# Optimization experiments

Hardware: AMD Instinct MI355X
Metric: run time of the kernel (lower is better)

## Reference

```python
import jax, jax.numpy as jnp
import numpy as np


def _safe_sqrt(x):
    # cdist-style euclidean distance with grad-safe sqrt at 0
    return jnp.sqrt(jnp.maximum(x, 1e-12))


def setup_inputs() -> dict:
    key = jax.random.key(0)
    k1, k2, k3 = jax.random.split(key, 3)
    B, P, D, C, N = 256, 196, 768, 15, 12544
    return {
        "query_features": jax.random.normal(k1, (B, P, D), dtype=jnp.float32),
        "keys": jax.random.normal(k2, (C, P, D), dtype=jnp.float32),
        "embeddings": jax.random.normal(k3, (N, D), dtype=jnp.float32),
        "num_samples": 196,
    }


def _retrieve_key(query_features, keys):
    # torch.cdist(new_flat.unsqueeze(1), keys_flat.unsqueeze(0)).squeeze(1); min over classes
    B = query_features.shape[0]
    C = keys.shape[0]
    q = query_features.reshape(B, -1)  # [B, P*D]
    k = keys.reshape(C, -1)            # [C, P*D]
    sq = (jnp.sum(q * q, axis=1)[:, None]
          + jnp.sum(k * k, axis=1)[None, :]
          - 2.0 * (q @ k.T))           # [B, C] squared distances via GEMM
    d = _safe_sqrt(sq)
    min_dist = jnp.min(d, axis=1)
    min_idx = jnp.argmin(d, axis=1)
    return min_dist, min_idx


def _fps(embeddings, num_samples):
    # furthest_point_sampling_embeddings: iterative cdist-to-last-centroid,
    # running min of distances, argmax picks next centroid.
    # (torch version seeds with a random index; we use index 0 deterministically)
    N = embeddings.shape[0]
    sqn = jnp.sum(embeddings * embeddings, axis=1)  # [N]

    def step(carry, _):
        dists, last = carry
        c = embeddings[last]                          # [D]
        cur = _safe_sqrt(sqn - 2.0 * (embeddings @ c) + jnp.sum(c * c))
        dists = jnp.minimum(dists, cur)
        nxt = jnp.argmax(dists).astype(jnp.int32)
        return (dists, nxt), nxt

    init = (jnp.full((N,), jnp.inf, dtype=embeddings.dtype), jnp.int32(0))
    _, idxs = jax.lax.scan(step, init, None, length=num_samples - 1)
    idxs = jnp.concatenate([jnp.zeros((1,), dtype=idxs.dtype), idxs])
    return embeddings[idxs]  # [num_samples, D]


def reference(query_features, keys, embeddings, num_samples):
    min_dist, min_idx = _retrieve_key(query_features, keys)
    samples = _fps(embeddings, num_samples)
    return min_dist, min_idx, samples
```

## Files before the change

kernel.cpp:

```cpp
#include <hip/hip_runtime.h>
#include <math.h>

typedef unsigned long long u64;
typedef unsigned int u32;

#define L_TOT  150528
#define ROW4   37632
#define NCHUNK 7
#define CH4    5376
#define R_ITERS 84
#define NBT    32
#define BTILE  8
#define NCLS   15

#define N_E    12544
#define DIM    768
#define NBLK   256
#define PPB    49
#define NSAMP  196
#define EPB    (PPB*DIM)
#define RSTRIDE 16

__device__ __forceinline__ float wave_sum(float v) {
#pragma unroll
  for (int m = 1; m < 64; m <<= 1) v += __shfl_xor(v, m, 64);
  return v;
}

__device__ __forceinline__ u64 wave_max_u64(u64 v) {
#pragma unroll
  for (int m = 1; m < 64; m <<= 1) {
    u64 o = __shfl_xor(v, m, 64);
    if (o > v) v = o;
  }
  return v;
}

__global__ __launch_bounds__(256) void retrieve_partial(
    const float* __restrict__ q, const float* __restrict__ k,
    float* __restrict__ part, float* __restrict__ kkpart) {
  const int bt = blockIdx.x;
  const int lc = blockIdx.y;
  const int tid = threadIdx.x;
  const int w = tid >> 6, lane = tid & 63;
  const int cbase = w * 4;
  const int ccnt = (w == 3) ? 3 : 4;
  const float4* qf = (const float4*)q;
  const float4* kf = (const float4*)k;
  const int fbase = lc * CH4 + lane;

  float acc[BTILE][4];
  float qq[BTILE];
  float kkv[4];
#pragma unroll
  for (int b = 0; b < BTILE; ++b) {
    qq[b] = 0.f;
#pragma unroll
    for (int c = 0; c < 4; ++c) acc[b][c] = 0.f;
  }
#pragma unroll
  for (int c = 0; c < 4; ++c) kkv[c] = 0.f;

  for (int it = 0; it < R_ITERS; ++it) {
    const int f = fbase + it * 64;
    float4 kv[4];
#pragma unroll
    for (int c = 0; c < 4; ++c)
      if (c < ccnt) kv[c] = kf[(size_t)(cbase + c) * ROW4 + f];
    if (bt == 0) {
#pragma unroll
      for (int c = 0; c < 4; ++c)
        if (c < ccnt)
          kkv[c] += kv[c].x*kv[c].x + kv[c].y*kv[c].y + kv[c].z*kv[c].z + kv[c].w*kv[c].w;
    }
#pragma unroll
    for (int b = 0; b < BTILE; ++b) {
      float4 qv = qf[(size_t)(bt * BTILE + b) * ROW4 + f];
#pragma unroll
      for (int c = 0; c < 4; ++c)
        if (c < ccnt)
          acc[b][c] += qv.x*kv[c].x + qv.y*kv[c].y + qv.z*kv[c].z + qv.w*kv[c].w;
      if (w == 3)
        qq[b] += qv.x*qv.x + qv.y*qv.y + qv.z*qv.z + qv.w*qv.w;
    }
  }

  const size_t pb = (size_t)(lc * NBT + bt) * 16;
#pragma unroll
  for (int b = 0; b < BTILE; ++b) {
#pragma unroll
    for (int c = 0; c < 4; ++c) {
      float v = wave_sum(acc[b][c]);
      if (lane == 0 && c < ccnt) part[(pb + cbase + c) * 8 + b] = v;
    }
    if (w == 3) {
      float v = wave_sum(qq[b]);
      if (lane == 0) part[(pb + 15) * 8 + b] = v;
    }
  }
  if (bt == 0) {
#pragma unroll
    for (int c = 0; c < 4; ++c) {
      float v = wave_sum(kkv[c]);
      if (lane == 0 && c < ccnt) kkpart[lc * 16 + cbase + c] = v;
    }
  }
}

__global__ __launch_bounds__(256) void retrieve_reduce(
    const float* __restrict__ part, const float* __restrict__ kkpart,
    float* __restrict__ out) {
  __shared__ float kn[NCLS];
  const int t = threadIdx.x;
  if (t < NCLS) {
    float s = 0.f;
    for (int lc = 0; lc < NCHUNK; ++lc) s += kkpart[lc * 16 + t];
    kn[t] = s;
  }
  __syncthreads();
  const int bt = t >> 3, bi = t & 7;
  float qq = 0.f;
  for (int lc = 0; lc < NCHUNK; ++lc)
    qq += part[((size_t)(lc * NBT + bt) * 16 + 15) * 8 + bi];
  float dmin = INFINITY;
  int didx = 0;
  for (int c = 0; c < NCLS; ++c) {
    float dot = 0.f;
    for (int lc = 0; lc < NCHUNK; ++lc)
      dot += part[((size_t)(lc * NBT + bt) * 16 + c) * 8 + bi];
    float d2 = qq + kn[c] - 2.f * dot;
    float d = sqrtf(fmaxf(d2, 1e-12f));
    if (d < dmin) { dmin = d; didx = c; }
  }
  out[t] = dmin;
  out[256 + t] = (float)didx;
}

__global__ __launch_bounds__(1024, 4) void fps_kernel(
    const float* __restrict__ emb,
    u64* __restrict__ words,
    u64* __restrict__ res8,
    float* __restrict__ out_samples) {
  extern __shared__ float e_lds[];
  const int tid = threadIdx.x;
  const int blk = blockIdx.x;
  const int w = tid >> 6, lane = tid & 63;
  const int q4 = lane >> 4;
  const int r = lane & 15;
  const int pl = w * 4 + q4;
  const bool valid = pl < PPB;
  const int p = valid ? pl : 0;

  __shared__ int hist[NSAMP];
  __shared__ u64 wkey[16];
  __shared__ u64 swin[4];

  {
    const float* src = emb + (size_t)blk * EPB;
    for (int i = tid; i < EPB; i += 1024) e_lds[i] = src[i];
  }
  __syncthreads();

  const float4* ef = (const float4*)(e_lds + (size_t)p * DIM);
  float sq;
  {
    float ss = 0.f;
#pragma unroll
    for (int jj = 0; jj < 12; ++jj) {
      float4 v = ef[r + jj * 16];
      ss = fmaf(v.x, v.x, ss); ss = fmaf(v.y, v.y, ss);
      ss = fmaf(v.z, v.z, ss); ss = fmaf(v.w, v.w, ss);
    }
#pragma unroll
    for (int m = 1; m < 16; m <<= 1) ss += __shfl_xor(ss, m, 64);
    sq = ss;
  }
  float dist2 = INFINITY;
  int last = 0;
  if (tid == 0) hist[0] = 0;
  __syncthreads();

  for (int s = 1; s < NSAMP; ++s) {
    const int buf = (s & 1) * NBLK;

    const float4* cf = (const float4*)(emb + (size_t)last * DIM);
    float4 cv[12];
#pragma unroll
    for (int jj = 0; jj < 12; ++jj) cv[jj] = cf[r + jj * 16];

    float a = 0.f, cn = 0.f;
#pragma unroll
    for (int jj = 0; jj < 12; ++jj) {
      float4 e4 = ef[r + jj * 16];
      float4 c4 = cv[jj];
      a = fmaf(e4.x, c4.x, a); a = fmaf(e4.y, c4.y, a);
      a = fmaf(e4.z, c4.z, a); a = fmaf(e4.w, c4.w, a);
      cn = fmaf(c4.x, c4.x, cn); cn = fmaf(c4.y, c4.y, cn);
      cn = fmaf(c4.z, c4.z, cn); cn = fmaf(c4.w, c4.w, cn);
    }
#pragma unroll
    for (int m = 1; m < 16; m <<= 1) {
      a += __shfl_xor(a, m, 64);
      cn += __shfl_xor(cn, m, 64);
    }

    u64 key = 0ull;
    if (valid) {
      float d2 = sq - 2.f * a + cn;
      if (d2 < dist2) dist2 = d2;
      key = ((u64)__float_as_uint(dist2) << 32) |
            (u32)(~(u32)(blk * PPB + pl));
    }
#pragma unroll
    for (int m = 16; m < 64; m <<= 1) {
      u64 o = __shfl_xor(key, m, 64);
      if (o > key) key = o;
    }
    if (lane == 0) wkey[w] = key;
    __syncthreads();

    if (w == 0) {
      u64 k = wkey[lane & 15];
#pragma unroll
      for (int m = 1; m < 16; m <<= 1) {
        u64 o = __shfl_xor(k, m, 64);
        if (o > k) k = o;
      }
      if (lane == 0) {
        const u32 bidx = ~(u32)(k & 0xffffffffull);
        const u32 bdist = (u32)(k >> 32);
        const u64 word = ((u64)s << 48) | ((u64)bdist << 16) | (u64)bidx;
        __hip_atomic_store(&words[buf + blk], word, __ATOMIC_RELAXED,
                           __HIP_MEMORY_SCOPE_AGENT);
      }
    }

    if (blk == 0) {
      if (tid < NBLK) {
        u64 w64;
        for (;;) {
          w64 = __hip_atomic_load(&words[buf + tid], __ATOMIC_RELAXED,
                                  __HIP_MEMORY_SCOPE_AGENT);
          if ((w64 >> 48) >= (u64)s) break;
        }
        u64 kk = (((w64 >> 16) & 0xffffffffull) << 32) |
                 (u64)(u32)(~(u32)(w64 & 0xffffull));
        kk = wave_max_u64(kk);
        if (lane == 0) swin[w] = kk;
      }
      __syncthreads();
      if (tid == 0) {
        u64 m = swin[0];
#pragma unroll
        for (int qi = 1; qi < 4; ++qi) if (swin[qi] > m) m = swin[qi];
        const int widx = (int)(~(u32)(m & 0xffffffffull));
        hist[s] = widx;
        const u64 rw = ((u64)s << 32) | (u32)widx;
#pragma unroll
        for (int c = 0; c < 8; ++c)
          __hip_atomic_store(&res8[(size_t)c * RSTRIDE], rw,
                             __ATOMIC_RELAXED, __HIP_MEMORY_SCOPE_AGENT);
      }
      __syncthreads();
    } else {
      if (tid == 0) {
        const u64* rp = &res8[(size_t)(blk & 7) * RSTRIDE];
        u64 r0, r1, r2, r3, rr;
        for (;;) {
          r0 = __hip_atomic_load(rp, __ATOMIC_RELAXED,
                                 __HIP_MEMORY_SCOPE_AGENT);
          r1 = __hip_atomic_load(rp, __ATOMIC_RELAXED,
                                 __HIP_MEMORY_SCOPE_AGENT);
          r2 = __hip_atomic_load(rp, __ATOMIC_RELAXED,
                                 __HIP_MEMORY_SCOPE_AGENT);
          r3 = __hip_atomic_load(rp, __ATOMIC_RELAXED,
                                 __HIP_MEMORY_SCOPE_AGENT);
          if ((r3 >> 32) >= (u64)s) { rr = r3; break; }
          if ((r2 >> 32) >= (u64)s) { rr = r2; break; }
          if ((r1 >> 32) >= (u64)s) { rr = r1; break; }
          if ((r0 >> 32) >= (u64)s) { rr = r0; break; }
        }
        hist[s] = (int)(u32)(rr & 0xffffffffull);
      }
      __syncthreads();
    }
    last = hist[s];
  }

  if (blk < NSAMP) {
    const int idx = hist[blk];
    const float4* src = (const float4*)(emb + (size_t)idx * DIM);
    float4* dst = (float4*)(out_samples + (size_t)blk * DIM);
    if (tid < DIM / 4) dst[tid] = src[tid];
  }
}

extern "C" void kernel_launch(void* const* d_in, const int* in_sizes, int n_in,
                              void* d_out, int out_size, void* d_ws, size_t ws_size,
                              hipStream_t stream) {
  const float* q   = (const float*)d_in[0];
  const float* k   = (const float*)d_in[1];
  const float* emb = (const float*)d_in[2];
  float* out = (float*)d_out;

  u64* words = (u64*)d_ws;
  u64* res8  = (u64*)((char*)d_ws + 4096);
  float* part   = (float*)((char*)d_ws + 8192);
  float* kkpart = part + 28672;

  hipMemsetAsync(d_ws, 0, 8192, stream);

  hipLaunchKernelGGL(retrieve_partial, dim3(NBT, NCHUNK), dim3(256), 0, stream,
                     q, k, part, kkpart);
  hipLaunchKernelGGL(retrieve_reduce, dim3(1), dim3(256), 0, stream,
                     part, kkpart, out);

  hipFuncSetAttribute((const void*)fps_kernel,
                      hipFuncAttributeMaxDynamicSharedMemorySize,
                      EPB * sizeof(float));

  float* samples = out + 512;
  void* args[] = {(void*)&emb, (void*)&words, (void*)&res8, (void*)&samples};
  hipLaunchCooperativeKernel((void*)fps_kernel, dim3(NBLK), dim3(1024), args,
                             EPB * sizeof(float), stream);
}
```

Baseline: 872.2 us.

## Replace per-step workgroup barriers in FPS with sequence-tagged LDS flag polling

```diff
diff --git a/kernel.cpp b/kernel.cpp
--- a/kernel.cpp
+++ b/kernel.cpp
@@ -34,6 +34,17 @@
     if (o > v) v = o;
   }
   return v;
+}
+
+__device__ __forceinline__ u64 key_from_word(u64 w) {
+  return (((w >> 16) & 0xffffffffull) << 32) |
+         (u64)(u32)(~(u32)(w & 0xffffull));
+}
+
+__device__ __forceinline__ u64 word_from_key(u64 s, u64 k) {
+  const u32 bidx = ~(u32)(k & 0xffffffffull);
+  const u32 bdist = (u32)(k >> 32);
+  return (s << 48) | ((u64)bdist << 16) | (u64)bidx;
 }
 
 __global__ __launch_bounds__(256) void retrieve_partial(
@@ -152,12 +163,21 @@
   const int p = valid ? pl : 0;
 
   __shared__ int hist[NSAMP];
-  __shared__ u64 wkey[16];
-  __shared__ u64 swin[4];
+  __shared__ u64 wkey[2][16];
+  __shared__ u64 swin[2][4];
+  __shared__ u64 lres[2];
 
   {
     const float* src = emb + (size_t)blk * EPB;
     for (int i = tid; i < EPB; i += 1024) e_lds[i] = src[i];
+  }
+  if (tid == 0) {
+    hist[0] = 0;
+#pragma unroll
+    for (int i = 0; i < 16; ++i) { wkey[0][i] = 0ull; wkey[1][i] = 0ull; }
+#pragma unroll
+    for (int i = 0; i < 4; ++i) { swin[0][i] = 0ull; swin[1][i] = 0ull; }
+    lres[0] = 0ull; lres[1] = 0ull;
   }
   __syncthreads();
 
@@ -177,11 +197,10 @@
   }
   float dist2 = INFINITY;
   int last = 0;
-  if (tid == 0) hist[0] = 0;
-  __syncthreads();
 
   for (int s = 1; s < NSAMP; ++s) {
-    const int buf = (s & 1) * NBLK;
+    const int par = s & 1;
+    const int buf = par * NBLK;
 
     const float4* cf = (const float4*)(emb + (size_t)last * DIM);
     float4 cv[12];
@@ -216,23 +235,30 @@
       u64 o = __shfl_xor(key, m, 64);
       if (o > key) key = o;
     }
-    if (lane == 0) wkey[w] = key;
-    __syncthreads();
+
+    if (lane == 0)
+      __hip_atomic_store(&wkey[par][w], word_from_key((u64)s, key),
+                         __ATOMIC_RELAXED, __HIP_MEMORY_SCOPE_WORKGROUP);
 
     if (w == 0) {
-      u64 k = wkey[lane & 15];
+      u64 kw = 0ull;
+      if (lane < 16) {
+        u64 t64;
+        for (;;) {
+          t64 = __hip_atomic_load(&wkey[par][lane], __ATOMIC_RELAXED,
+                                  __HIP_MEMORY_SCOPE_WORKGROUP);
+          if ((t64 >> 48) >= (u64)s) break;
+        }
+        kw = key_from_word(t64);
+      }
 #pragma unroll
       for (int m = 1; m < 16; m <<= 1) {
-        u64 o = __shfl_xor(k, m, 64);
-        if (o > k) k = o;
-      }
-      if (lane == 0) {
-        const u32 bidx = ~(u32)(k & 0xffffffffull);
-        const u32 bdist = (u32)(k >> 32);
-        const u64 word = ((u64)s << 48) | ((u64)bdist << 16) | (u64)bidx;
-        __hip_atomic_store(&words[buf + blk], word, __ATOMIC_RELAXED,
-                           __HIP_MEMORY_SCOPE_AGENT);
-      }
+        u64 o = __shfl_xor(kw, m, 64);
+        if (o > kw) kw = o;
+      }
+      if (lane == 0)
+        __hip_atomic_store(&words[buf + blk], word_from_key((u64)s, kw),
+                           __ATOMIC_RELAXED, __HIP_MEMORY_SCOPE_AGENT);
     }
 
     if (blk == 0) {
@@ -243,25 +269,39 @@
                                   __HIP_MEMORY_SCOPE_AGENT);
           if ((w64 >> 48) >= (u64)s) break;
         }
-        u64 kk = (((w64 >> 16) & 0xffffffffull) << 32) |
-                 (u64)(u32)(~(u32)(w64 & 0xffffull));
-        kk = wave_max_u64(kk);
-        if (lane == 0) swin[w] = kk;
-      }
-      __syncthreads();
-      if (tid == 0) {
-        u64 m = swin[0];
-#pragma unroll
-        for (int qi = 1; qi < 4; ++qi) if (swin[qi] > m) m = swin[qi];
-        const int widx = (int)(~(u32)(m & 0xffffffffull));
-        hist[s] = widx;
+        u64 kk = wave_max_u64(key_from_word(w64));
+        if (lane == 0)
+          __hip_atomic_store(&swin[par][w], word_from_key((u64)s, kk),
+                             __ATOMIC_RELAXED, __HIP_MEMORY_SCOPE_WORKGROUP);
+      }
+      if (w == 0) {
+        u64 sw = 0ull;
+        if (lane < 4) {
+          u64 t64;
+          for (;;) {
+            t64 = __hip_atomic_load(&swin[par][lane], __ATOMIC_RELAXED,
+                                    __HIP_MEMORY_SCOPE_WORKGROUP);
+            if ((t64 >> 48) >= (u64)s) break;
+          }
+          sw = key_from_word(t64);
+        }
+#pragma unroll
+        for (int m = 1; m < 4; m <<= 1) {
+          u64 o = __shfl_xor(sw, m, 64);
+          if (o > sw) sw = o;
+        }
+        const u64 fin = __shfl(sw, 0, 64);
+        const int widx = (int)(~(u32)(fin & 0xffffffffull));
         const u64 rw = ((u64)s << 32) | (u32)widx;
-#pragma unroll
-        for (int c = 0; c < 8; ++c)
-          __hip_atomic_store(&res8[(size_t)c * RSTRIDE], rw,
+        if (lane < 8)
+          __hip_atomic_store(&res8[(size_t)lane * RSTRIDE], rw,
                              __ATOMIC_RELAXED, __HIP_MEMORY_SCOPE_AGENT);
-      }
-      __syncthreads();
+        if (lane == 0) {
+          hist[s] = widx;
+          __hip_atomic_store(&lres[par], rw, __ATOMIC_RELAXED,
+                             __HIP_MEMORY_SCOPE_WORKGROUP);
+        }
+      }
     } else {
       if (tid == 0) {
         const u64* rp = &res8[(size_t)(blk & 7) * RSTRIDE];
@@ -281,12 +321,21 @@
           if ((r0 >> 32) >= (u64)s) { rr = r0; break; }
         }
         hist[s] = (int)(u32)(rr & 0xffffffffull);
-      }
-      __syncthreads();
-    }
-    last = hist[s];
-  }
-
+        __hip_atomic_store(&lres[par], rr, __ATOMIC_RELAXED,
+                           __HIP_MEMORY_SCOPE_WORKGROUP);
+      }
+    }
+
+    u64 lr;
+    for (;;) {
+      lr = __hip_atomic_load(&lres[par], __ATOMIC_RELAXED,
+                             __HIP_MEMORY_SCOPE_WORKGROUP);
+      if ((lr >> 32) >= (u64)s) break;
+    }
+    last = (int)(u32)(lr & 0xffffffffull);
+  }
+
+  __syncthreads();
   if (blk < NSAMP) {
     const int idx = hist[blk];
     const float4* src = (const float4*)(emb + (size_t)idx * DIM);
```

New measurement: 909.0 us. 4.2% more time.
